# Optimization experiments

Hardware: AMD Instinct MI355X
Metric: run time of the kernel (lower is better)

Reference implementation:

```python
import jax, jax.numpy as jnp
import numpy as np


def setup_inputs() -> dict:
    key = jax.random.key(0)
    k1, k2 = jax.random.split(key)
    B, TOTAL_BITS, H, W = 16, 64, 128, 128
    C_OUT, N_BITS = 64, 4
    # binary bit-plane input, values in {0, 1}
    x = (jax.random.uniform(k1, (B, TOTAL_BITS, H, W)) < 0.5).astype(jnp.float32)
    # random bit-selection map: which input bit feeds each (out_channel, bit_pos)
    rp_map = jax.random.randint(k2, (C_OUT, N_BITS), 0, TOTAL_BITS)
    return {"x": x, "rp_map": rp_map}


def reference(x, rp_map):
    # bit_select_mode path of RPLayer.forward:
    #   gather n_bits_per_out random bits per output channel, then
    #   bit-pack with power-of-two weights (MAC-free projection).
    B, TB, H, W = x.shape
    C, nb = rp_map.shape
    # [B, TB, H, W] -> [B*H*W, TB]
    x_flat = x.transpose(0, 2, 3, 1).reshape(B * H * W, TB)
    # gather: [B*H*W, C, nb]  (fancy-index along bit axis, no expand needed)
    gathered = x_flat[:, rp_map]
    # power-of-two pack weights [1, 2, 4, 8, ...]
    pack_w = 2.0 ** jnp.arange(nb, dtype=x.dtype)
    packed = jnp.einsum('ncb,b->nc', gathered, pack_w)  # [B*H*W, C]
    # [B, H, W, C] -> [B, C, H, W]
    return packed.reshape(B, H, W, C).transpose(0, 3, 1, 2)
```

## Files before the change

kernel.cpp:

```cpp
#include <hip/hip_runtime.h>
#include <cstdint>
#include <cstddef>

constexpr int Bn = 16;
constexpr int TBn = 64;
constexpr int Cn = 64;
constexpr int HW = 128 * 128;
constexpr int TOTAL_PIX = Bn * HW;
constexpr int PIX_PER_BLOCK = 256;
constexpr int BLOCKS = TOTAL_PIX / PIX_PER_BLOCK;
constexpr int MROW = 20;

typedef float v4f __attribute__((ext_vector_type(4)));

__global__ __launch_bounds__(256) void rp_pack_nt(
    const float* __restrict__ x,
    const int* __restrict__ rp,
    float* __restrict__ out)
{
    __shared__ int4 s_rp[Cn];
    __shared__ unsigned short m16[64 * MROW];

    if (threadIdx.x < Cn) {
        s_rp[threadIdx.x] = reinterpret_cast<const int4*>(rp)[threadIdx.x];
    }

    const int b = blockIdx.x >> 6;
    const int pix0 = (blockIdx.x & 63) << 8;
    const int g = threadIdx.x & 63;
    const int q = threadIdx.x >> 6;

    const float* xb = x + (size_t)b * TBn * HW + (size_t)(q * 16) * HW + pix0 + g * 4;

    uint32_t p0 = 0, p1 = 0, p2 = 0, p3 = 0;
    #pragma unroll
    for (int i = 0; i < 16; ++i) {
        const v4f v = __builtin_nontemporal_load(
            reinterpret_cast<const v4f*>(xb + (size_t)i * HW));
        p0 |= ((__float_as_uint(v.x) >> 23) & 1u) << i;
        p1 |= ((__float_as_uint(v.y) >> 23) & 1u) << i;
        p2 |= ((__float_as_uint(v.z) >> 23) & 1u) << i;
        p3 |= ((__float_as_uint(v.w) >> 23) & 1u) << i;
    }

    unsigned short* row = &m16[g * MROW];
    row[0 * 4 + q] = (unsigned short)p0;
    row[1 * 4 + q] = (unsigned short)p1;
    row[2 * 4 + q] = (unsigned short)p2;
    row[3 * 4 + q] = (unsigned short)p3;

    __syncthreads();

    const uint64_t m0 = *reinterpret_cast<const uint64_t*>(&row[0]);
    const uint64_t m1 = *reinterpret_cast<const uint64_t*>(&row[4]);
    const uint64_t m2 = *reinterpret_cast<const uint64_t*>(&row[8]);
    const uint64_t m3 = *reinterpret_cast<const uint64_t*>(&row[12]);

    const int c0 = q * 16;
    float* ob = out + (size_t)b * Cn * HW + (size_t)c0 * HW + pix0 + g * 4;

    #pragma unroll
    for (int ci = 0; ci < 16; ++ci) {
        const int4 r = s_rp[c0 + ci];
        const unsigned i0 = (unsigned)r.x;
        const unsigned i1 = (unsigned)r.y;
        const unsigned i2 = (unsigned)r.z;
        const unsigned i3 = (unsigned)r.w;

        float4 o;
        o.x = (float)((unsigned)((m0 >> i0) & 1ull)
                    | ((unsigned)((m0 >> i1) & 1ull) << 1)
                    | ((unsigned)((m0 >> i2) & 1ull) << 2)
                    | ((unsigned)((m0 >> i3) & 1ull) << 3));
        o.y = (float)((unsigned)((m1 >> i0) & 1ull)
                    | ((unsigned)((m1 >> i1) & 1ull) << 1)
                    | ((unsigned)((m1 >> i2) & 1ull) << 2)
                    | ((unsigned)((m1 >> i3) & 1ull) << 3));
        o.z = (float)((unsigned)((m2 >> i0) & 1ull)
                    | ((unsigned)((m2 >> i1) & 1ull) << 1)
                    | ((unsigned)((m2 >> i2) & 1ull) << 2)
                    | ((unsigned)((m2 >> i3) & 1ull) << 3));
        o.w = (float)((unsigned)((m3 >> i0) & 1ull)
                    | ((unsigned)((m3 >> i1) & 1ull) << 1)
                    | ((unsigned)((m3 >> i2) & 1ull) << 2)
                    | ((unsigned)((m3 >> i3) & 1ull) << 3));

        *reinterpret_cast<float4*>(ob + (size_t)ci * HW) = o;
    }
}

extern "C" void kernel_launch(void* const* d_in, const int* in_sizes, int n_in,
                              void* d_out, int out_size, void* d_ws, size_t ws_size,
                              hipStream_t stream) {
    const float* x = (const float*)d_in[0];
    const int* rp = (const int*)d_in[1];
    float* out = (float*)d_out;

    constexpr int BLOCK = 256;
    rp_pack_nt<<<BLOCKS, BLOCK, 0, stream>>>(x, rp, out);
}
```

Before: 30.43 us.

## Split fused gather-pack into two kernels via packed bitmask workspace

Splits the single kernel into two launches. The first reads the input bit-planes and writes 64-bit packed bitmasks to a workspace buffer. The second reads those masks, transposes them in registers and writes the float outputs, replacing the shared-memory exchange and the intra-block barrier between the read and write phases. Nontemporal loads are also replaced with ordinary loads. This costs an extra kernel launch and a small global round trip in exchange for removing the barrier and letting each phase be scheduled separately.

```diff
diff --git a/kernel.cpp b/kernel.cpp
--- a/kernel.cpp
+++ b/kernel.cpp
@@ -7,57 +7,73 @@
 constexpr int Cn = 64;
 constexpr int HW = 128 * 128;
 constexpr int TOTAL_PIX = Bn * HW;
+constexpr int GROUPS = TOTAL_PIX / 4;
 constexpr int PIX_PER_BLOCK = 256;
 constexpr int BLOCKS = TOTAL_PIX / PIX_PER_BLOCK;
-constexpr int MROW = 20;
 
 typedef float v4f __attribute__((ext_vector_type(4)));
 
-__global__ __launch_bounds__(256) void rp_pack_nt(
+__global__ __launch_bounds__(256) void rp_pack_p1(
     const float* __restrict__ x,
-    const int* __restrict__ rp,
-    float* __restrict__ out)
+    uint64_t* __restrict__ ws)
 {
-    __shared__ int4 s_rp[Cn];
-    __shared__ unsigned short m16[64 * MROW];
-
-    if (threadIdx.x < Cn) {
-        s_rp[threadIdx.x] = reinterpret_cast<const int4*>(rp)[threadIdx.x];
-    }
-
     const int b = blockIdx.x >> 6;
     const int pix0 = (blockIdx.x & 63) << 8;
     const int g = threadIdx.x & 63;
     const int q = threadIdx.x >> 6;
 
-    const float* xb = x + (size_t)b * TBn * HW + (size_t)(q * 16) * HW + pix0 + g * 4;
+    const float* xb = x + (size_t)b * TBn * HW + (size_t)(q * 16) * HW
+                        + pix0 + g * 4;
 
     uint32_t p0 = 0, p1 = 0, p2 = 0, p3 = 0;
     #pragma unroll
     for (int i = 0; i < 16; ++i) {
-        const v4f v = __builtin_nontemporal_load(
-            reinterpret_cast<const v4f*>(xb + (size_t)i * HW));
+        const v4f v = *reinterpret_cast<const v4f*>(xb + (size_t)i * HW);
         p0 |= ((__float_as_uint(v.x) >> 23) & 1u) << i;
         p1 |= ((__float_as_uint(v.y) >> 23) & 1u) << i;
         p2 |= ((__float_as_uint(v.z) >> 23) & 1u) << i;
         p3 |= ((__float_as_uint(v.w) >> 23) & 1u) << i;
     }
 
-    unsigned short* row = &m16[g * MROW];
-    row[0 * 4 + q] = (unsigned short)p0;
-    row[1 * 4 + q] = (unsigned short)p1;
-    row[2 * 4 + q] = (unsigned short)p2;
-    row[3 * 4 + q] = (unsigned short)p3;
+    const uint64_t v64 = (uint64_t)(unsigned short)p0
+                       | ((uint64_t)(unsigned short)p1 << 16)
+                       | ((uint64_t)(unsigned short)p2 << 32)
+                       | ((uint64_t)(unsigned short)p3 << 48);
+    ws[(size_t)q * GROUPS + blockIdx.x * 64 + g] = v64;
+}
 
+__global__ __launch_bounds__(256) void rp_pack_p2(
+    const uint64_t* __restrict__ ws,
+    const int* __restrict__ rp,
+    float* __restrict__ out)
+{
+    __shared__ int4 s_rp[Cn];
+    if (threadIdx.x < Cn) {
+        s_rp[threadIdx.x] = reinterpret_cast<const int4*>(rp)[threadIdx.x];
+    }
     __syncthreads();
 
-    const uint64_t m0 = *reinterpret_cast<const uint64_t*>(&row[0]);
-    const uint64_t m1 = *reinterpret_cast<const uint64_t*>(&row[4]);
-    const uint64_t m2 = *reinterpret_cast<const uint64_t*>(&row[8]);
-    const uint64_t m3 = *reinterpret_cast<const uint64_t*>(&row[12]);
+    const int gg = blockIdx.x * 64 + (threadIdx.x & 63);
+    const int cq = threadIdx.x >> 6;
 
-    const int c0 = q * 16;
-    float* ob = out + (size_t)b * Cn * HW + (size_t)c0 * HW + pix0 + g * 4;
+    const uint64_t r0 = ws[gg];
+    const uint64_t r1 = ws[(size_t)GROUPS + gg];
+    const uint64_t r2 = ws[(size_t)2 * GROUPS + gg];
+    const uint64_t r3 = ws[(size_t)3 * GROUPS + gg];
+
+    const uint64_t m0 = ((r0      ) & 0xffffull)        | (((r1      ) & 0xffffull) << 16)
+                      | (((r2      ) & 0xffffull) << 32) | (((r3      ) & 0xffffull) << 48);
+    const uint64_t m1 = ((r0 >> 16) & 0xffffull)        | (((r1 >> 16) & 0xffffull) << 16)
+                      | (((r2 >> 16) & 0xffffull) << 32) | (((r3 >> 16) & 0xffffull) << 48);
+    const uint64_t m2 = ((r0 >> 32) & 0xffffull)        | (((r1 >> 32) & 0xffffull) << 16)
+                      | (((r2 >> 32) & 0xffffull) << 32) | (((r3 >> 32) & 0xffffull) << 48);
+    const uint64_t m3 = ((r0 >> 48) & 0xffffull)        | (((r1 >> 48) & 0xffffull) << 16)
+                      | (((r2 >> 48) & 0xffffull) << 32) | (((r3 >> 48) & 0xffffull) << 48);
+
+    const int b = gg >> 12;
+    const int pix = (gg & 4095) << 2;
+    const int c0 = cq * 16;
+    float* ob = out + (size_t)b * Cn * HW + (size_t)c0 * HW + pix;
 
     #pragma unroll
     for (int ci = 0; ci < 16; ++ci) {
@@ -95,7 +111,9 @@
     const float* x = (const float*)d_in[0];
     const int* rp = (const int*)d_in[1];
     float* out = (float*)d_out;
+    uint64_t* ws = (uint64_t*)d_ws;
 
     constexpr int BLOCK = 256;
-    rp_pack_nt<<<BLOCKS, BLOCK, 0, stream>>>(x, rp, out);
+    rp_pack_p1<<<BLOCKS, BLOCK, 0, stream>>>(x, ws);
+    rp_pack_p2<<<BLOCKS, BLOCK, 0, stream>>>(ws, rp, out);
 }
```

Measured after the change: 31.39 us. 1.03x slower.
